# Kernel tuning notes

Hardware: AMD Instinct MI355X
Metric: run time of the kernel (lower is better)

The kernel has to match this reference:

```python
import jax, jax.numpy as jnp
import numpy as np

SEQ_LEN = 4096
D_IN = 2048
D_OUT = 2048
DROPOUT_P = 0.5


def setup_inputs() -> dict:
    key = jax.random.key(0)
    kx, kq, kk, kv = jax.random.split(key, 4)
    return {
        "x": jax.random.normal(kx, (SEQ_LEN, D_IN), dtype=jnp.float32),
        "W_query": jax.random.uniform(kq, (D_IN, D_OUT), dtype=jnp.float32),
        "W_key": jax.random.uniform(kk, (D_IN, D_OUT), dtype=jnp.float32),
        "W_value": jax.random.uniform(kv, (D_IN, D_OUT), dtype=jnp.float32),
    }


def reference(x, W_query, W_key, W_value):
    # projections: [S, d_in] @ [d_in, d_out] -> [S, d_out]
    queries = x @ W_query
    keys = x @ W_key
    values = x @ W_value
    # full score matrix [S, S]
    attn_scores = queries @ keys.T
    S = attn_scores.shape[0]
    causal_mask = jnp.triu(jnp.ones((S, S), dtype=bool), k=1)
    masked = jnp.where(causal_mask, -jnp.inf, attn_scores)
    scale = jnp.sqrt(jnp.asarray(keys.shape[-1], dtype=masked.dtype))
    attn_weights = jax.nn.softmax(masked / scale, axis=1)
    # dropout p=0.5 (train mode), inverted scaling, deterministic key
    keep = jax.random.bernoulli(jax.random.key(42), 1.0 - DROPOUT_P, attn_weights.shape)
    attn_weights = jnp.where(keep, attn_weights / (1.0 - DROPOUT_P), 0.0)
    context_vec = attn_weights @ values  # [S, d_out]
    return context_vec
```

## Files before the change

kernel.cpp:

```cpp
#include <hip/hip_runtime.h>
#include <cstdint>
#include <cstddef>
#include <cmath>

#define SEQ 4096
#define DM  2048

typedef unsigned int u32;
typedef unsigned short u16;
typedef __attribute__((ext_vector_type(8))) short bf16x8;
typedef __attribute__((ext_vector_type(4))) float f32x4;
typedef __attribute__((ext_vector_type(16))) float f32x16;

__device__ __forceinline__ u16 f2bf(float f) {
  u32 u = __float_as_uint(f);
  return (u16)((u + 0x7FFFu + ((u >> 16) & 1u)) >> 16);
}
__device__ __forceinline__ float bf2f(u16 h) { return __uint_as_float(((u32)h) << 16); }

__device__ __forceinline__ u32 rotl32(u32 x, int r) { return (x << r) | (x >> (32 - r)); }

__device__ __forceinline__ void tf2x32(u32 c0, u32 c1, u32& o0, u32& o1) {
  const u32 k0 = 0u, k1 = 42u, k2 = 0x1BD11BDAu ^ 0u ^ 42u;
  u32 x0 = c0 + k0;
  u32 x1 = c1 + k1;
#define TFR(r) { x0 += x1; x1 = rotl32(x1, (r)); x1 ^= x0; }
  TFR(13) TFR(15) TFR(26) TFR(6)   x0 += k1; x1 += k2 + 1u;
  TFR(17) TFR(29) TFR(16) TFR(24)  x0 += k2; x1 += k0 + 2u;
  TFR(13) TFR(15) TFR(26) TFR(6)   x0 += k0; x1 += k1 + 3u;
  TFR(17) TFR(29) TFR(16) TFR(24)  x0 += k1; x1 += k2 + 4u;
  TFR(13) TFR(15) TFR(26) TFR(6)   x0 += k2; x1 += k0 + 5u;
#undef TFR
  o0 = x0; o1 = x1;
}

__device__ __forceinline__ bool dropout_keep(u32 idx) {
  u32 a, b; tf2x32(0u, idx, a, b);
  return (((a ^ b) & 0x80000000u) == 0u);
}

__device__ __forceinline__ void g2l16(const void* g, void* l) {
  __builtin_amdgcn_global_load_lds((const __attribute__((address_space(1))) u32*)g,
                                   (__attribute__((address_space(3))) u32*)l, 16, 0, 0);
}

#define MFMA16(a, b, c) __builtin_amdgcn_mfma_f32_16x16x32_bf16(a, b, c, 0, 0, 0)
#define MFMA32(a, b, c) __builtin_amdgcn_mfma_f32_32x32x16_bf16(a, b, c, 0, 0, 0)


__device__ __forceinline__ void gemm_core(
    const u16* __restrict__ Ah, const u16* __restrict__ Bh,
    int lda, int ldb, int rowBlock, int colBlock, int kmax,
    f32x4 (&acc)[4][4], u16* smem)
{
  u16* Als = smem;
  u16* Bls = smem + 8192;
  const int tid  = threadIdx.x;
  const int wid  = tid >> 6;
  const int lane = tid & 63;
  const int wr   = (wid & 1) << 6;
  const int wc   = (wid >> 1) << 6;
  const int lrow = lane & 15;
  const int lk   = (((lane >> 4) ^ ((lrow >> 1) & 3)) << 3);
  const int srow = wid * 32 + (lane >> 2);
  const int skol = (((lane & 3) ^ ((lane >> 3) & 3)) << 3);

  const f32x4 zero = {0.f, 0.f, 0.f, 0.f};
#pragma unroll
  for (int i = 0; i < 4; ++i)
#pragma unroll
    for (int j = 0; j < 4; ++j) acc[i][j] = zero;

  for (int kb = 0; kb < kmax; kb += 64) {
#pragma unroll
    for (int h = 0; h < 2; ++h)
#pragma unroll
      for (int t = 0; t < 2; ++t) {
        const size_t ga = (size_t)(rowBlock + srow + t * 16) * lda + kb + h * 32 + skol;
        const size_t gb = (size_t)(colBlock + srow + t * 16) * ldb + kb + h * 32 + skol;
        const int lo = h * 4096 + (wid * 32 + t * 16) * 32;
        g2l16(Ah + ga, &Als[lo]);
        g2l16(Bh + gb, &Bls[lo]);
      }
    __syncthreads();

#pragma unroll
    for (int h = 0; h < 2; ++h) {
      bf16x8 ah[4], bh[4];
#pragma unroll
      for (int r = 0; r < 4; ++r) {
        ah[r] = *(const bf16x8*)&Als[h * 4096 + (wr + r * 16 + lrow) * 32 + lk];
        bh[r] = *(const bf16x8*)&Bls[h * 4096 + (wc + r * 16 + lrow) * 32 + lk];
      }
#pragma unroll
      for (int r = 0; r < 4; ++r)
#pragma unroll
        for (int c = 0; c < 4; ++c)
          acc[r][c] = MFMA16(ah[r], bh[c], acc[r][c]);
    }
    __syncthreads();
  }
}

__global__ __launch_bounds__(256) void k_split_all(
    const float* __restrict__ X, u16* __restrict__ Xh, u16* __restrict__ Xl,
    const float* __restrict__ Wq, const float* __restrict__ Wk, const float* __restrict__ Wv,
    u16* __restrict__ Wqh, u16* __restrict__ Wql,
    u16* __restrict__ Wkh, u16* __restrict__ Wkl, u16* __restrict__ Wvh) {
  __shared__ float t[64][65];
  const int bid = blockIdx.x;
  const int tid = threadIdx.x;
  const int wid = tid >> 6, lane = tid & 63;

  if (bid < 4096) {
    const int kt16 = bid & 127;
    const int rt32 = (bid >> 7) * 4 + wid;
    const int row = rt32 * 32 + (lane & 31);
    const int col = kt16 * 16 + ((lane >> 5) << 3);
    const float* src = X + (size_t)row * DM + col;
    const float4 v0 = *(const float4*)src;
    const float4 v1 = *(const float4*)(src + 4);
    float v[8] = {v0.x, v0.y, v0.z, v0.w, v1.x, v1.y, v1.z, v1.w};
    u16 h[8], l[8];
#pragma unroll
    for (int j = 0; j < 8; ++j) {
      h[j] = f2bf(v[j]);
      l[j] = f2bf(v[j] - bf2f(h[j]));
    }
    u16* hp = Xh + (size_t)row * DM + col;
    *(ushort4*)hp = *(ushort4*)&h[0];
    *(ushort4*)(hp + 4) = *(ushort4*)&h[4];
    u16* lp = Xl + (((size_t)rt32 * 128 + kt16) * 64 + lane) * 8;
    *(ushort4*)lp = *(ushort4*)&l[0];
    *(ushort4*)(lp + 4) = *(ushort4*)&l[4];
    return;
  }

  const int r = bid - 4096;
  const int z = r >> 10;
  const int rem = r & 1023;
  const int n0 = (rem & 31) * 64, k0 = (rem >> 5) * 64;
  const float* W = (z == 0) ? Wq : (z == 1) ? Wk : Wv;
  u16* Oh = (z == 0) ? Wqh : (z == 1) ? Wkh : Wvh;
  u16* Ol = (z == 0) ? Wql : Wkl;
  const int tx = tid & 63, ty = tid >> 6;
#pragma unroll
  for (int i = 0; i < 16; ++i)
    t[ty * 16 + i][tx] = W[(size_t)(k0 + ty * 16 + i) * DM + n0 + tx];
  __syncthreads();
  {
    const int nl = tid >> 2, kc = (tid & 3) * 16;
    u16 h[16];
#pragma unroll
    for (int i = 0; i < 16; ++i) h[i] = f2bf(t[kc + i][nl]);
    u16* hp = Oh + (size_t)(n0 + nl) * DM + k0 + kc;
#pragma unroll
    for (int i = 0; i < 4; ++i) *(ushort4*)(hp + i * 4) = *(ushort4*)&h[i * 4];
  }
  if (z < 2) {
#pragma unroll
    for (int tt = 0; tt < 2; ++tt) {
      const int idx = wid * 2 + tt;
      const int rt = idx >> 2, kt = idx & 3;
      const int nl = rt * 32 + (lane & 31);
      const int kc = kt * 16 + ((lane >> 5) << 3);
      u16 l[8];
#pragma unroll
      for (int j = 0; j < 8; ++j) {
        const float v = t[kc + j][nl];
        l[j] = f2bf(v - bf2f(f2bf(v)));
      }
      const int rtg = (n0 >> 5) + rt, ktg = (k0 >> 4) + kt;
      u16* lp = Ol + (((size_t)rtg * (DM / 16) + ktg) * 64 + lane) * 8;
      *(ushort4*)lp = *(ushort4*)&l[0];
      *(ushort4*)(lp + 4) = *(ushort4*)&l[4];
    }
  }
}

__global__ __launch_bounds__(512, 2) void k_proj_qk(
    const u16* __restrict__ Xh, const u16* __restrict__ Xl,
    const u16* __restrict__ Wqh, const u16* __restrict__ Wql,
    const u16* __restrict__ Wkh, const u16* __restrict__ Wkl,
    u16* __restrict__ Qh, u16* __restrict__ Ql,
    u16* __restrict__ Kh, u16* __restrict__ Kl, float rscaleQ)
{
  __shared__ __align__(16) u16 smem[65536];
  const int z = blockIdx.z;
  const u16* __restrict__ Bw = z ? Wkh : Wqh;
  const u16* __restrict__ Bl = z ? Wkl : Wql;
  u16* __restrict__ Oh = z ? Kh : Qh;
  u16* __restrict__ Ol = z ? Kl : Ql;
  const float rs = z ? 1.0f : rscaleQ;

  const int rowBlock = blockIdx.y * 256;
  const int colBlock = blockIdx.x * 256;
  const int tid  = threadIdx.x;
  const int wid  = tid >> 6, lane = tid & 63;
  const int wm   = wid >> 2, wn = wid & 3;
  const int l31  = lane & 31, lh = lane >> 5;
  const int srow = tid >> 2, schunk = tid & 3;
  const int sko  = ((schunk ^ ((srow >> 1) & 3)) << 3);
  const int rkey = (l31 >> 1) & 3;

  f32x16 acc[4][2];
  {
    const f32x16 z16 = {0.f,0.f,0.f,0.f,0.f,0.f,0.f,0.f,0.f,0.f,0.f,0.f,0.f,0.f,0.f,0.f};
#pragma unroll
    for (int r = 0; r < 4; ++r)
#pragma unroll
      for (int c = 0; c < 2; ++c) acc[r][c] = z16;
  }

#define P_STG_AHI(pp) g2l16(Xh + (size_t)(rowBlock + (pp)*128 + srow) * DM + kbn + sko, \
                            &smem[bufN + (pp)*4096 + tid*8]);
#define P_STG_BHI(pp) g2l16(Bw + (size_t)(colBlock + (pp)*128 + srow) * DM + kbn + sko, \
                            &smem[bufN + 8192 + (pp)*4096 + tid*8]);
#define P_STG_ALO(ss) { const int idx_ = (ss)*8 + wid; \
    g2l16(Xl + ((size_t)((rowBlock >> 5) + (idx_ >> 1)) * 128 + (kbn >> 4) + (idx_ & 1)) * 512 + lane*8, \
          &smem[bufN + 16384 + idx_*512 + lane*8]); }
#define P_STG_BLO(ss) { const int idx_ = (ss)*8 + wid; \
    g2l16(Bl + ((size_t)((colBlock >> 5) + (idx_ >> 1)) * 128 + (kbn >> 4) + (idx_ & 1)) * 512 + lane*8, \
          &smem[bufN + 24576 + idx_*512 + lane*8]); }

#define P_PHASE(qq) { \
    bf16x8 ah[4], bh[2], al[4], bl[2]; \
    const int cl_ = (qq)*2 + lh; \
    _Pragma("unroll") for (int r_ = 0; r_ < 4; ++r_) \
      ah[r_] = *(const bf16x8*)&smem[bufC + ((wm*128 + r_*32 + l31) << 5) + ((cl_ ^ rkey) << 3)]; \
    _Pragma("unroll") for (int c_ = 0; c_ < 2; ++c_) \
      bh[c_] = *(const bf16x8*)&smem[bufC + 8192 + ((wn*64 + c_*32 + l31) << 5) + ((cl_ ^ rkey) << 3)]; \
    _Pragma("unroll") for (int r_ = 0; r_ < 4; ++r_) \
      al[r_] = *(const bf16x8*)&smem[bufC + 16384 + ((wm*4 + r_)*2 + (qq))*512 + lane*8]; \
    _Pragma("unroll") for (int c_ = 0; c_ < 2; ++c_) \
      bl[c_] = *(const bf16x8*)&smem[bufC + 24576 + ((wn*2 + c_)*2 + (qq))*512 + lane*8]; \
    __builtin_amdgcn_s_setprio(1); \
    _Pragma("unroll") for (int r_ = 0; r_ < 4; ++r_) \
      _Pragma("unroll") for (int c_ = 0; c_ < 2; ++c_) { \
        acc[r_][c_] = MFMA32(ah[r_], bh[c_], acc[r_][c_]); \
        acc[r_][c_] = MFMA32(ah[r_], bl[c_], acc[r_][c_]); \
        acc[r_][c_] = MFMA32(al[r_], bh[c_], acc[r_][c_]); } \
    __builtin_amdgcn_s_setprio(0); }

  {
    const size_t kbn = 0; const int bufN = 0;
    P_STG_AHI(0) P_STG_AHI(1) P_STG_BHI(0) P_STG_BHI(1)
    P_STG_ALO(0) P_STG_ALO(1) P_STG_BLO(0) P_STG_BLO(1)
  }
  asm volatile("s_waitcnt vmcnt(0)" ::: "memory");
  __builtin_amdgcn_s_barrier();

  for (int t = 0; t < 64; ++t) {
    const int bufC = (t & 1) << 15;
    const int bufN = bufC ^ 32768;
    const size_t kbn = (size_t)(t + 1) * 32;
    if (t < 63) { P_STG_AHI(0) P_STG_AHI(1) P_STG_BHI(0) P_STG_BHI(1) }
    __builtin_amdgcn_sched_barrier(0);
    P_PHASE(0)
    if (t < 63) { P_STG_ALO(0) P_STG_ALO(1) P_STG_BLO(0) P_STG_BLO(1) }
    __builtin_amdgcn_sched_barrier(0);
    P_PHASE(1)
    asm volatile("s_waitcnt vmcnt(0)" ::: "memory");
    __builtin_amdgcn_s_barrier();
  }
#undef P_PHASE
#undef P_STG_BLO
#undef P_STG_ALO
#undef P_STG_BHI
#undef P_STG_AHI

  __syncthreads();
  u16* scr = smem + wid * 8192;
  const int r0g = rowBlock + wm * 128;
  const int c0g = colBlock + wn * 64;
#pragma unroll
  for (int r = 0; r < 4; ++r)
#pragma unroll
    for (int c = 0; c < 2; ++c) {
      const int colL = c * 32 + l31;
#pragma unroll
      for (int g = 0; g < 4; ++g)
#pragma unroll
        for (int e = 0; e < 4; ++e) {
          const int rowL = r * 32 + 8 * g + 4 * lh + e;
          const float v = acc[r][c][g * 4 + e] * rs;
          const u16 h = f2bf(v);
          Oh[(size_t)(r0g + rowL) * DM + c0g + colL] = h;
          scr[rowL * 64 + (((colL >> 3) ^ (rowL & 7)) << 3) + (colL & 7)] =
              f2bf(v - bf2f(h));
        }
    }
  asm volatile("s_waitcnt lgkmcnt(0)" ::: "memory");
  __builtin_amdgcn_sched_barrier(0);
#pragma unroll
  for (int rt = 0; rt < 4; ++rt)
#pragma unroll
    for (int kt = 0; kt < 4; ++kt) {
      const int rowL = rt * 32 + l31;
      const int cl2 = kt * 2 + lh;
      const bf16x8 v = *(const bf16x8*)&scr[rowL * 64 + ((cl2 ^ (rowL & 7)) << 3)];
      const int rtg = (rowBlock >> 5) + wm * 4 + rt;
      const int ktg = (colBlock >> 4) + wn * 4 + kt;
      *(bf16x8*)(Ol + (((size_t)rtg * 128 + ktg) * 64 + lane) * 8) = v;
    }
}

__global__ __launch_bounds__(512, 2) void k_proj_v(
    const u16* __restrict__ Xh, const u16* __restrict__ Wvh, u16* __restrict__ Vt)
{
  __shared__ __align__(16) u16 smem[49152];
  const int rowBlock = blockIdx.y * 256;
  const int colBlock = blockIdx.x * 128;
  const int tid  = threadIdx.x;
  const int wid  = tid >> 6, lane = tid & 63;
  const int wm   = wid >> 1, wn = wid & 1;
  const int l31  = lane & 31, lh = lane >> 5;
  const int srow = tid >> 2, schunk = tid & 3;
  const int sko  = ((schunk ^ ((srow >> 1) & 3)) << 3);
  const int rkey = (l31 >> 1) & 3;

  f32x16 acc[2][2];
  {
    const f32x16 z16 = {0.f,0.f,0.f,0.f,0.f,0.f,0.f,0.f,0.f,0.f,0.f,0.f,0.f,0.f,0.f,0.f};
#pragma unroll
    for (int r = 0; r < 2; ++r)
#pragma unroll
      for (int c = 0; c < 2; ++c) acc[r][c] = z16;
  }

#define V_STGA(hh, pp) g2l16(Xh + (size_t)(rowBlock + (pp)*128 + srow) * DM + kbn + (hh)*32 + sko, \
                             &smem[bufN + (hh)*8192 + (pp)*4096 + tid*8]);
#define V_STGB(hh)     g2l16(Wvh + (size_t)(colBlock + srow) * DM + kbn + (hh)*32 + sko, \
                             &smem[bufN + 16384 + (hh)*4096 + tid*8]);

#define V_PH(qq, STMT) { \
    __builtin_amdgcn_sched_barrier(0); \
    STMT; \
    bf16x8 ah[2], bh[2]; \
    const int cl_ = ((qq) & 1) * 2 + lh; \
    const int hx_ = (qq) >> 1; \
    _Pragma("unroll") for (int r_ = 0; r_ < 2; ++r_) \
      ah[r_] = *(const bf16x8*)&smem[bufC + ((hx_*256 + wm*64 + r_*32 + l31) << 5) + ((cl_ ^ rkey) << 3)]; \
    _Pragma("unroll") for (int c_ = 0; c_ < 2; ++c_) \
      bh[c_] = *(const bf16x8*)&smem[bufC + 16384 + ((hx_*128 + wn*64 + c_*32 + l31) << 5) + ((cl_ ^ rkey) << 3)]; \
    __builtin_amdgcn_s_setprio(1); \
    _Pragma("unroll") for (int r_ = 0; r_ < 2; ++r_) \
      _Pragma("unroll") for (int c_ = 0; c_ < 2; ++c_) \
        acc[r_][c_] = MFMA32(ah[r_], bh[c_], acc[r_][c_]); \
    __builtin_amdgcn_s_setprio(0); }

  {
    const size_t kbn = 0; const int bufN = 0;
    V_STGA(0,0) V_STGA(0,1) V_STGA(1,0) V_STGA(1,1) V_STGB(0) V_STGB(1)
  }
  asm volatile("s_waitcnt vmcnt(0)" ::: "memory");
  __builtin_amdgcn_s_barrier();

  for (int t = 0; t < 32; ++t) {
    const int bufC = (t & 1) * 24576;
    const int bufN = bufC ^ 24576;
    const size_t kbn = (size_t)(t + 1) * 64;
    const bool more = (t < 31);
    V_PH(0, if (more) { V_STGA(0,0) V_STGA(0,1) V_STGB(0) })
    V_PH(1, if (more) { V_STGA(1,0) V_STGA(1,1) V_STGB(1) })
    V_PH(2, ;)
    V_PH(3, ;)
    asm volatile("s_waitcnt vmcnt(0)" ::: "memory");
    __builtin_amdgcn_s_barrier();
  }
#undef V_PH
#undef V_STGB
#undef V_STGA

  const int vr0 = rowBlock + wm * 64;
#pragma unroll
  for (int r = 0; r < 2; ++r)
#pragma unroll
    for (int c = 0; c < 2; ++c) {
      const int col = colBlock + wn * 64 + c * 32 + l31;
#pragma unroll
      for (int g = 0; g < 4; ++g) {
        ushort4 pk;
        pk.x = f2bf(acc[r][c][g * 4 + 0]);
        pk.y = f2bf(acc[r][c][g * 4 + 1]);
        pk.z = f2bf(acc[r][c][g * 4 + 2]);
        pk.w = f2bf(acc[r][c][g * 4 + 3]);
        *(ushort4*)(Vt + (size_t)col * SEQ + vr0 + r * 32 + 8 * g + 4 * lh) = pk;
      }
    }
}

__global__ __launch_bounds__(512, 2) void k_scores(
    const u16* __restrict__ Qh, const u16* __restrict__ Ql,
    const u16* __restrict__ Kh, const u16* __restrict__ Kl, float* __restrict__ S)
{
  __shared__ __align__(16) u16 smem[49152];
  const int bid = blockIdx.x;
  int by = (int)((sqrtf(4.0f * (float)bid + 1.0f) - 1.0f) * 0.5f);
  while ((by + 1) * (by + 2) <= bid) ++by;
  while (by * (by + 1) > bid) --by;
  const int bx = bid - by * (by + 1);
  const int rowBlock = by * 256, colBlock = bx * 128;

  const int tid  = threadIdx.x;
  const int wid  = tid >> 6, lane = tid & 63;
  const int wm   = wid >> 1, wn = wid & 1;
  const int l31  = lane & 31, lh = lane >> 5;
  const int srow = tid >> 2, schunk = tid & 3;
  const int sko  = ((schunk ^ ((srow >> 1) & 3)) << 3);
  const int rkey = (l31 >> 1) & 3;

  f32x16 acc[2][2];
  {
    const f32x16 z16 = {0.f,0.f,0.f,0.f,0.f,0.f,0.f,0.f,0.f,0.f,0.f,0.f,0.f,0.f,0.f,0.f};
#pragma unroll
    for (int r = 0; r < 2; ++r)
#pragma unroll
      for (int c = 0; c < 2; ++c) acc[r][c] = z16;
  }

#define S_STG_AHI(pp) g2l16(Qh + (size_t)(rowBlock + (pp)*128 + srow) * DM + kbn + sko, \
                            &smem[bufN + (pp)*4096 + tid*8]);
#define S_STG_BHI     g2l16(Kh + (size_t)(colBlock + srow) * DM + kbn + sko, \
                            &smem[bufN + 8192 + tid*8]);
#define S_STG_ALO(ss) { const int idx_ = (ss)*8 + wid; \
    g2l16(Ql + ((size_t)((rowBlock >> 5) + (idx_ >> 1)) * 128 + (kbn >> 4) + (idx_ & 1)) * 512 + lane*8, \
          &smem[bufN + 12288 + idx_*512 + lane*8]); }
#define S_STG_BLO     { const int idx_ = wid; \
    g2l16(Kl + ((size_t)((colBlock >> 5) + (idx_ >> 1)) * 128 + (kbn >> 4) + (idx_ & 1)) * 512 + lane*8, \
          &smem[bufN + 20480 + idx_*512 + lane*8]); }

#define S_PHASE(qq) { \
    bf16x8 ah[2], bh[2], al[2], bl[2]; \
    const int cl_ = (qq)*2 + lh; \
    _Pragma("unroll") for (int r_ = 0; r_ < 2; ++r_) \
      ah[r_] = *(const bf16x8*)&smem[bufC + ((wm*64 + r_*32 + l31) << 5) + ((cl_ ^ rkey) << 3)]; \
    _Pragma("unroll") for (int c_ = 0; c_ < 2; ++c_) \
      bh[c_] = *(const bf16x8*)&smem[bufC + 8192 + ((wn*64 + c_*32 + l31) << 5) + ((cl_ ^ rkey) << 3)]; \
    _Pragma("unroll") for (int r_ = 0; r_ < 2; ++r_) \
      al[r_] = *(const bf16x8*)&smem[bufC + 12288 + ((wm*2 + r_)*2 + (qq))*512 + lane*8]; \
    _Pragma("unroll") for (int c_ = 0; c_ < 2; ++c_) \
      bl[c_] = *(const bf16x8*)&smem[bufC + 20480 + ((wn*2 + c_)*2 + (qq))*512 + lane*8]; \
    __builtin_amdgcn_s_setprio(1); \
    _Pragma("unroll") for (int r_ = 0; r_ < 2; ++r_) \
      _Pragma("unroll") for (int c_ = 0; c_ < 2; ++c_) { \
        acc[r_][c_] = MFMA32(ah[r_], bh[c_], acc[r_][c_]); \
        acc[r_][c_] = MFMA32(ah[r_], bl[c_], acc[r_][c_]); \
        acc[r_][c_] = MFMA32(al[r_], bh[c_], acc[r_][c_]); } \
    __builtin_amdgcn_s_setprio(0); }

  {
    const size_t kbn = 0; const int bufN = 0;
    S_STG_AHI(0) S_STG_AHI(1) S_STG_BHI
    S_STG_ALO(0) S_STG_ALO(1) S_STG_BLO
  }
  asm volatile("s_waitcnt vmcnt(0)" ::: "memory");
  __builtin_amdgcn_s_barrier();

  for (int t = 0; t < 64; ++t) {
    const int bufC = (t & 1) * 24576;
    const int bufN = bufC ^ 24576;
    const size_t kbn = (size_t)(t + 1) * 32;
    if (t < 63) { S_STG_AHI(0) S_STG_AHI(1) S_STG_BHI }
    __builtin_amdgcn_sched_barrier(0);
    S_PHASE(0)
    if (t < 63) { S_STG_ALO(0) S_STG_ALO(1) S_STG_BLO }
    __builtin_amdgcn_sched_barrier(0);
    S_PHASE(1)
    asm volatile("s_waitcnt vmcnt(0)" ::: "memory");
    __builtin_amdgcn_s_barrier();
  }
#undef S_PHASE
#undef S_STG_BLO
#undef S_STG_ALO
#undef S_STG_BHI
#undef S_STG_AHI

  const int r0 = rowBlock + wm * 64, c0 = colBlock + wn * 64;
#pragma unroll
  for (int r = 0; r < 2; ++r)
#pragma unroll
    for (int c = 0; c < 2; ++c) {
      const int col = c0 + c * 32 + l31;
#pragma unroll
      for (int g = 0; g < 4; ++g)
#pragma unroll
        for (int e = 0; e < 4; ++e) {
          const int row = r0 + r * 32 + 8 * g + 4 * lh + e;
          S[(size_t)row * SEQ + col] = acc[r][c][g * 4 + e];
        }
    }
}

__global__ __launch_bounds__(256) void k_softmax_dropout(const float* __restrict__ S,
                                                         u16* __restrict__ P) {
  const int row = blockIdx.x;
  const int n = row + 1;
  const int nt = (n + 1023) >> 10;
  const int tid = threadIdx.x;
  __shared__ float buf[SEQ];
  __shared__ float red[4];
  __shared__ float bcast;
  const float* srow = S + (size_t)row * SEQ;

  float lmax = -INFINITY;
  for (int t = 0; t < nt; ++t) {
    int j4 = tid + t * 256;
    float4 v = *(const float4*)(srow + (size_t)j4 * 4);
    int b = j4 * 4;
    float x0 = (b + 0 < n) ? v.x : -INFINITY;
    float x1 = (b + 1 < n) ? v.y : -INFINITY;
    float x2 = (b + 2 < n) ? v.z : -INFINITY;
    float x3 = (b + 3 < n) ? v.w : -INFINITY;
    buf[b + 0] = x0; buf[b + 1] = x1; buf[b + 2] = x2; buf[b + 3] = x3;
    lmax = fmaxf(lmax, fmaxf(fmaxf(x0, x1), fmaxf(x2, x3)));
  }
  for (int off = 32; off > 0; off >>= 1) lmax = fmaxf(lmax, __shfl_down(lmax, off, 64));
  if ((tid & 63) == 0) red[tid >> 6] = lmax;
  __syncthreads();
  if (tid == 0) bcast = fmaxf(fmaxf(red[0], red[1]), fmaxf(red[2], red[3]));
  __syncthreads();
  const float m = bcast;

  float lsum = 0.f;
  for (int t = 0; t < nt; ++t) {
    int b = (tid + t * 256) * 4;
    float e0 = expf(buf[b + 0] - m);
    float e1 = expf(buf[b + 1] - m);
    float e2 = expf(buf[b + 2] - m);
    float e3 = expf(buf[b + 3] - m);
    buf[b + 0] = e0; buf[b + 1] = e1; buf[b + 2] = e2; buf[b + 3] = e3;
    lsum += (e0 + e1) + (e2 + e3);
  }
  for (int off = 32; off > 0; off >>= 1) lsum += __shfl_down(lsum, off, 64);
  if ((tid & 63) == 0) red[tid >> 6] = lsum;
  __syncthreads();
  if (tid == 0) bcast = (red[0] + red[1]) + (red[2] + red[3]);
  __syncthreads();
  const float total = bcast;

  u16* prow = P + (size_t)row * SEQ;
  const int zeroEnd = ((row >> 7) + 1) << 7;
  for (int j = tid; j < zeroEnd; j += 256) {
    float out = 0.f;
    if (j < n) {
      const float w = buf[j] / total;
      out = dropout_keep((u32)(row * SEQ + j)) ? w * 2.0f : 0.f;
    }
    prow[j] = f2bf(out);
  }
}

__global__ __launch_bounds__(256) void k_pv(const u16* __restrict__ P,
                                            const u16* __restrict__ Vt,
                                            float* __restrict__ O) {
  __shared__ __align__(16) u16 smem[16384];
  const int by = (SEQ / 128 - 1) - blockIdx.y;
  f32x4 acc[4][4];
  gemm_core(P, Vt, SEQ, SEQ, by * 128, blockIdx.x * 128, (by + 1) * 128, acc, smem);

  const int lane = threadIdx.x & 63, wid = threadIdx.x >> 6;
  const int r0 = by * 128 + ((wid & 1) << 6) + ((lane >> 4) << 2);
  const int c0 = blockIdx.x * 128 + ((wid >> 1) << 6) + (lane & 15);
#pragma unroll
  for (int r = 0; r < 4; ++r)
#pragma unroll
    for (int c = 0; c < 4; ++c)
#pragma unroll
      for (int e = 0; e < 4; ++e)
        O[(size_t)(r0 + r * 16 + e) * DM + (c0 + c * 16)] = acc[r][c][e];
}

extern "C" void kernel_launch(void* const* d_in, const int* in_sizes, int n_in,
                              void* d_out, int out_size, void* d_ws, size_t ws_size,
                              hipStream_t stream) {
  const float* x  = (const float*)d_in[0];
  const float* Wq = (const float*)d_in[1];
  const float* Wk = (const float*)d_in[2];
  const float* Wv = (const float*)d_in[3];

  const size_t PL = (size_t)SEQ * DM;
  const size_t WL = (size_t)DM * DM;
  u16* base = (u16*)d_ws;
  u16* Qh = base;
  u16* Ql = Qh + PL;
  u16* Kh = Ql + PL;
  u16* Kl = Kh + PL;
  u16* Vt = Kl + PL;
  u16* P  = base;
  u16* regA = Vt + PL;
  u16* Xh  = regA;
  u16* Xl  = Xh + PL;
  u16* Wqh = Xl + PL;
  u16* Wql = Wqh + WL;
  u16* Wkh = Wql + WL;
  u16* Wkl = Wkh + WL;
  u16* Wvh = Wkl + WL;
  float* S = (float*)regA;

  const float rscale = 1.0f / sqrtf(2048.0f);
  k_split_all<<<dim3(4096 + 3 * 1024), dim3(256), 0, stream>>>(
      x, Xh, Xl, Wq, Wk, Wv, Wqh, Wql, Wkh, Wkl, Wvh);
  k_proj_qk<<<dim3(DM / 256, SEQ / 256, 2), dim3(512), 0, stream>>>(
      Xh, Xl, Wqh, Wql, Wkh, Wkl, Qh, Ql, Kh, Kl, rscale);
  k_proj_v<<<dim3(DM / 128, SEQ / 256), dim3(512), 0, stream>>>(Xh, Wvh, Vt);
  k_scores<<<dim3(272), dim3(512), 0, stream>>>(Qh, Ql, Kh, Kl, S);
  k_softmax_dropout<<<dim3(SEQ), dim3(256), 0, stream>>>(S, P);
  k_pv<<<dim3(DM / 128, SEQ / 128), dim3(256), 0, stream>>>(P, Vt, (float*)d_out);
}
```

Before: 610.4 us.

## Split K-tile loads by phase and use partial vmcnt waits in GEMMs

Reorganizes the global-to-LDS staging in the projection and score GEMM main loops. Each tile's loads are grouped by which MFMA phase consumes them, and each phase waits with a partial vmcnt count plus a barrier instead of draining all loads at the end of the iteration. The last iteration is peeled. The aim is to let phase 0 compute start before the phase-1 low-part loads arrive, keeping more loads in flight. In exchange there are more barriers per iteration, and the hardcoded vmcnt counts depend on exact issue order, so correctness is fragile.

```diff
diff --git a/kernel.cpp b/kernel.cpp
--- a/kernel.cpp
+++ b/kernel.cpp
@@ -212,16 +212,20 @@
       for (int c = 0; c < 2; ++c) acc[r][c] = z16;
   }
 
-#define P_STG_AHI(pp) g2l16(Xh + (size_t)(rowBlock + (pp)*128 + srow) * DM + kbn + sko, \
-                            &smem[bufN + (pp)*4096 + tid*8]);
-#define P_STG_BHI(pp) g2l16(Bw + (size_t)(colBlock + (pp)*128 + srow) * DM + kbn + sko, \
-                            &smem[bufN + 8192 + (pp)*4096 + tid*8]);
-#define P_STG_ALO(ss) { const int idx_ = (ss)*8 + wid; \
-    g2l16(Xl + ((size_t)((rowBlock >> 5) + (idx_ >> 1)) * 128 + (kbn >> 4) + (idx_ & 1)) * 512 + lane*8, \
-          &smem[bufN + 16384 + idx_*512 + lane*8]); }
-#define P_STG_BLO(ss) { const int idx_ = (ss)*8 + wid; \
-    g2l16(Bl + ((size_t)((colBlock >> 5) + (idx_ >> 1)) * 128 + (kbn >> 4) + (idx_ & 1)) * 512 + lane*8, \
-          &smem[bufN + 24576 + idx_*512 + lane*8]); }
+#define QK_G1 { \
+    g2l16(Xh + (size_t)(rowBlock + srow) * DM + kbn + sko,          &smem[bufN + tid*8]); \
+    g2l16(Xh + (size_t)(rowBlock + 128 + srow) * DM + kbn + sko,    &smem[bufN + 4096 + tid*8]); \
+    g2l16(Bw + (size_t)(colBlock + srow) * DM + kbn + sko,          &smem[bufN + 8192 + tid*8]); \
+    g2l16(Bw + (size_t)(colBlock + 128 + srow) * DM + kbn + sko,    &smem[bufN + 12288 + tid*8]); \
+    g2l16(Xl + ((size_t)((rowBlock >> 5) + wid) * 128 + (kbn >> 4)) * 512 + lane*8, \
+          &smem[bufN + 16384 + (wid*2)*512 + lane*8]); \
+    g2l16(Bl + ((size_t)((colBlock >> 5) + wid) * 128 + (kbn >> 4)) * 512 + lane*8, \
+          &smem[bufN + 24576 + (wid*2)*512 + lane*8]); }
+#define QK_G2 { \
+    g2l16(Xl + ((size_t)((rowBlock >> 5) + wid) * 128 + (kbn >> 4) + 1) * 512 + lane*8, \
+          &smem[bufN + 16384 + (wid*2+1)*512 + lane*8]); \
+    g2l16(Bl + ((size_t)((colBlock >> 5) + wid) * 128 + (kbn >> 4) + 1) * 512 + lane*8, \
+          &smem[bufN + 24576 + (wid*2+1)*512 + lane*8]); }
 
 #define P_PHASE(qq) { \
     bf16x8 ah[4], bh[2], al[4], bl[2]; \
@@ -244,30 +248,40 @@
 
   {
     const size_t kbn = 0; const int bufN = 0;
-    P_STG_AHI(0) P_STG_AHI(1) P_STG_BHI(0) P_STG_BHI(1)
-    P_STG_ALO(0) P_STG_ALO(1) P_STG_BLO(0) P_STG_BLO(1)
-  }
-  asm volatile("s_waitcnt vmcnt(0)" ::: "memory");
-  __builtin_amdgcn_s_barrier();
-
-  for (int t = 0; t < 64; ++t) {
+    QK_G1 QK_G2
+  }
+
+  for (int t = 0; t < 63; ++t) {
     const int bufC = (t & 1) << 15;
     const int bufN = bufC ^ 32768;
     const size_t kbn = (size_t)(t + 1) * 32;
-    if (t < 63) { P_STG_AHI(0) P_STG_AHI(1) P_STG_BHI(0) P_STG_BHI(1) }
-    __builtin_amdgcn_sched_barrier(0);
+    QK_G1
+    asm volatile("s_waitcnt vmcnt(8)" ::: "memory");
+    __builtin_amdgcn_s_barrier();
+    asm volatile("" ::: "memory");
     P_PHASE(0)
-    if (t < 63) { P_STG_ALO(0) P_STG_ALO(1) P_STG_BLO(0) P_STG_BLO(1) }
-    __builtin_amdgcn_sched_barrier(0);
+    QK_G2
+    asm volatile("s_waitcnt vmcnt(8)" ::: "memory");
+    __builtin_amdgcn_s_barrier();
+    asm volatile("" ::: "memory");
     P_PHASE(1)
+    asm volatile("" ::: "memory");
+    __builtin_amdgcn_s_barrier();
+  }
+  {
+    const int bufC = 32768;
+    asm volatile("s_waitcnt vmcnt(2)" ::: "memory");
+    __builtin_amdgcn_s_barrier();
+    asm volatile("" ::: "memory");
+    P_PHASE(0)
     asm volatile("s_waitcnt vmcnt(0)" ::: "memory");
     __builtin_amdgcn_s_barrier();
+    asm volatile("" ::: "memory");
+    P_PHASE(1)
   }
 #undef P_PHASE
-#undef P_STG_BLO
-#undef P_STG_ALO
-#undef P_STG_BHI
-#undef P_STG_AHI
+#undef QK_G2
+#undef QK_G1
 
   __syncthreads();
   u16* scr = smem + wid * 8192;
@@ -419,16 +433,19 @@
       for (int c = 0; c < 2; ++c) acc[r][c] = z16;
   }
 
-#define S_STG_AHI(pp) g2l16(Qh + (size_t)(rowBlock + (pp)*128 + srow) * DM + kbn + sko, \
-                            &smem[bufN + (pp)*4096 + tid*8]);
-#define S_STG_BHI     g2l16(Kh + (size_t)(colBlock + srow) * DM + kbn + sko, \
-                            &smem[bufN + 8192 + tid*8]);
-#define S_STG_ALO(ss) { const int idx_ = (ss)*8 + wid; \
-    g2l16(Ql + ((size_t)((rowBlock >> 5) + (idx_ >> 1)) * 128 + (kbn >> 4) + (idx_ & 1)) * 512 + lane*8, \
-          &smem[bufN + 12288 + idx_*512 + lane*8]); }
-#define S_STG_BLO     { const int idx_ = wid; \
-    g2l16(Kl + ((size_t)((colBlock >> 5) + (idx_ >> 1)) * 128 + (kbn >> 4) + (idx_ & 1)) * 512 + lane*8, \
-          &smem[bufN + 20480 + idx_*512 + lane*8]); }
+#define S_G1 { \
+    g2l16(Qh + (size_t)(rowBlock + srow) * DM + kbn + sko,        &smem[bufN + tid*8]); \
+    g2l16(Qh + (size_t)(rowBlock + 128 + srow) * DM + kbn + sko,  &smem[bufN + 4096 + tid*8]); \
+    g2l16(Kh + (size_t)(colBlock + srow) * DM + kbn + sko,        &smem[bufN + 8192 + tid*8]); \
+    g2l16(Ql + ((size_t)((rowBlock >> 5) + wid) * 128 + (kbn >> 4)) * 512 + lane*8, \
+          &smem[bufN + 12288 + (wid*2)*512 + lane*8]); \
+    g2l16(Kl + ((size_t)((colBlock >> 5) + (wid & 3)) * 128 + (kbn >> 4)) * 512 + lane*8, \
+          &smem[bufN + 20480 + ((wid & 3)*2)*512 + lane*8]); }
+#define S_G2 { \
+    g2l16(Ql + ((size_t)((rowBlock >> 5) + wid) * 128 + (kbn >> 4) + 1) * 512 + lane*8, \
+          &smem[bufN + 12288 + (wid*2+1)*512 + lane*8]); \
+    g2l16(Kl + ((size_t)((colBlock >> 5) + (wid & 3)) * 128 + (kbn >> 4) + 1) * 512 + lane*8, \
+          &smem[bufN + 20480 + ((wid & 3)*2+1)*512 + lane*8]); }
 
 #define S_PHASE(qq) { \
     bf16x8 ah[2], bh[2], al[2], bl[2]; \
@@ -451,30 +468,40 @@
 
   {
     const size_t kbn = 0; const int bufN = 0;
-    S_STG_AHI(0) S_STG_AHI(1) S_STG_BHI
-    S_STG_ALO(0) S_STG_ALO(1) S_STG_BLO
-  }
-  asm volatile("s_waitcnt vmcnt(0)" ::: "memory");
-  __builtin_amdgcn_s_barrier();
-
-  for (int t = 0; t < 64; ++t) {
+    S_G1 S_G2
+  }
+
+  for (int t = 0; t < 63; ++t) {
     const int bufC = (t & 1) * 24576;
     const int bufN = bufC ^ 24576;
     const size_t kbn = (size_t)(t + 1) * 32;
-    if (t < 63) { S_STG_AHI(0) S_STG_AHI(1) S_STG_BHI }
-    __builtin_amdgcn_sched_barrier(0);
+    S_G1
+    asm volatile("s_waitcnt vmcnt(7)" ::: "memory");
+    __builtin_amdgcn_s_barrier();
+    asm volatile("" ::: "memory");
     S_PHASE(0)
-    if (t < 63) { S_STG_ALO(0) S_STG_ALO(1) S_STG_BLO }
-    __builtin_amdgcn_sched_barrier(0);
+    S_G2
+    asm volatile("s_waitcnt vmcnt(7)" ::: "memory");
+    __builtin_amdgcn_s_barrier();
+    asm volatile("" ::: "memory");
     S_PHASE(1)
+    asm volatile("" ::: "memory");
+    __builtin_amdgcn_s_barrier();
+  }
+  {
+    const int bufC = 24576;
+    asm volatile("s_waitcnt vmcnt(2)" ::: "memory");
+    __builtin_amdgcn_s_barrier();
+    asm volatile("" ::: "memory");
+    S_PHASE(0)
     asm volatile("s_waitcnt vmcnt(0)" ::: "memory");
     __builtin_amdgcn_s_barrier();
+    asm volatile("" ::: "memory");
+    S_PHASE(1)
   }
 #undef S_PHASE
-#undef S_STG_BLO
-#undef S_STG_ALO
-#undef S_STG_BHI
-#undef S_STG_AHI
+#undef S_G2
+#undef S_G1
 
   const int r0 = rowBlock + wm * 64, c0 = colBlock + wn * 64;
 #pragma unroll
```

After: 634.7 us. 1.04x slower.

## Shrink QK projection and score tiles, stage K16 slices per warp with higher occupancy

Applied to the files above, without the earlier changes.

Tiles shrink in two kernels: the Q/K projection goes from 256x256 to 128x256 and the causal score kernel from 256x128 to 128x128, with the triangular block mapping recomputed for the new grid. Staging now uses per-warp pointers that advance through K in 16-wide steps with simple strided loads into unswizzled shared memory. This cuts shared memory per block and raises the occupancy hint (4 blocks per CU), aiming to hide latency better and reduce wasted work on the causal diagonal. The cost is less operand reuse per block, twice as many loop iterations with a barrier each, and possible bank conflicts, since the swizzling was dropped and high-part rows are now read with a plain lane stride.

```diff
diff --git a/kernel.cpp b/kernel.cpp
--- a/kernel.cpp
+++ b/kernel.cpp
@@ -178,103 +178,93 @@
   }
 }
 
-__global__ __launch_bounds__(512, 2) void k_proj_qk(
+__global__ __launch_bounds__(512, 4) void k_proj_qk(
     const u16* __restrict__ Xh, const u16* __restrict__ Xl,
     const u16* __restrict__ Wqh, const u16* __restrict__ Wql,
     const u16* __restrict__ Wkh, const u16* __restrict__ Wkl,
     u16* __restrict__ Qh, u16* __restrict__ Ql,
     u16* __restrict__ Kh, u16* __restrict__ Kl, float rscaleQ)
 {
-  __shared__ __align__(16) u16 smem[65536];
+  __shared__ __align__(16) u16 smem[32768];
   const int z = blockIdx.z;
   const u16* __restrict__ Bw = z ? Wkh : Wqh;
-  const u16* __restrict__ Bl = z ? Wkl : Wql;
+  const u16* __restrict__ Blg = z ? Wkl : Wql;
   u16* __restrict__ Oh = z ? Kh : Qh;
   u16* __restrict__ Ol = z ? Kl : Ql;
   const float rs = z ? 1.0f : rscaleQ;
 
-  const int rowBlock = blockIdx.y * 256;
+  const int rowBlock = blockIdx.y * 128;
   const int colBlock = blockIdx.x * 256;
   const int tid  = threadIdx.x;
   const int wid  = tid >> 6, lane = tid & 63;
   const int wm   = wid >> 2, wn = wid & 3;
   const int l31  = lane & 31, lh = lane >> 5;
-  const int srow = tid >> 2, schunk = tid & 3;
-  const int sko  = ((schunk ^ ((srow >> 1) & 3)) << 3);
-  const int rkey = (l31 >> 1) & 3;
-
-  f32x16 acc[4][2];
+
+  const u16* srcA;
+  size_t stepA;
+  if (wid < 4) {
+    srcA  = Xh + (size_t)(rowBlock + wid * 32 + l31) * DM + lh * 8;
+    stepA = 16;
+  } else {
+    srcA  = Xl + (size_t)((rowBlock >> 5) + (wid - 4)) * 128 * 512 + lane * 8;
+    stepA = 512;
+  }
+  const u16* srcBh = Bw  + (size_t)(colBlock + wid * 32 + l31) * DM + lh * 8;
+  const u16* srcBl = Blg + (size_t)((colBlock >> 5) + wid) * 128 * 512 + lane * 8;
+
+  f32x16 acc[2][2];
   {
     const f32x16 z16 = {0.f,0.f,0.f,0.f,0.f,0.f,0.f,0.f,0.f,0.f,0.f,0.f,0.f,0.f,0.f,0.f};
 #pragma unroll
-    for (int r = 0; r < 4; ++r)
+    for (int r = 0; r < 2; ++r)
 #pragma unroll
       for (int c = 0; c < 2; ++c) acc[r][c] = z16;
   }
 
-#define P_STG_AHI(pp) g2l16(Xh + (size_t)(rowBlock + (pp)*128 + srow) * DM + kbn + sko, \
-                            &smem[bufN + (pp)*4096 + tid*8]);
-#define P_STG_BHI(pp) g2l16(Bw + (size_t)(colBlock + (pp)*128 + srow) * DM + kbn + sko, \
-                            &smem[bufN + 8192 + (pp)*4096 + tid*8]);
-#define P_STG_ALO(ss) { const int idx_ = (ss)*8 + wid; \
-    g2l16(Xl + ((size_t)((rowBlock >> 5) + (idx_ >> 1)) * 128 + (kbn >> 4) + (idx_ & 1)) * 512 + lane*8, \
-          &smem[bufN + 16384 + idx_*512 + lane*8]); }
-#define P_STG_BLO(ss) { const int idx_ = (ss)*8 + wid; \
-    g2l16(Bl + ((size_t)((colBlock >> 5) + (idx_ >> 1)) * 128 + (kbn >> 4) + (idx_ & 1)) * 512 + lane*8, \
-          &smem[bufN + 24576 + idx_*512 + lane*8]); }
-
-#define P_PHASE(qq) { \
-    bf16x8 ah[4], bh[2], al[4], bl[2]; \
-    const int cl_ = (qq)*2 + lh; \
-    _Pragma("unroll") for (int r_ = 0; r_ < 4; ++r_) \
-      ah[r_] = *(const bf16x8*)&smem[bufC + ((wm*128 + r_*32 + l31) << 5) + ((cl_ ^ rkey) << 3)]; \
-    _Pragma("unroll") for (int c_ = 0; c_ < 2; ++c_) \
-      bh[c_] = *(const bf16x8*)&smem[bufC + 8192 + ((wn*64 + c_*32 + l31) << 5) + ((cl_ ^ rkey) << 3)]; \
-    _Pragma("unroll") for (int r_ = 0; r_ < 4; ++r_) \
-      al[r_] = *(const bf16x8*)&smem[bufC + 16384 + ((wm*4 + r_)*2 + (qq))*512 + lane*8]; \
-    _Pragma("unroll") for (int c_ = 0; c_ < 2; ++c_) \
-      bl[c_] = *(const bf16x8*)&smem[bufC + 24576 + ((wn*2 + c_)*2 + (qq))*512 + lane*8]; \
+#define P_STG(bufN) { \
+    g2l16(srcA,  &smem[(bufN) + tid * 8]); \
+    g2l16(srcBh, &smem[(bufN) + 4096 + tid * 8]); \
+    g2l16(srcBl, &smem[(bufN) + 8192 + tid * 8]); \
+    srcA += stepA; srcBh += 16; srcBl += 512; }
+
+#define P_PH(bufC) { \
+    bf16x8 ah[2], bh[2], al[2], bl[2]; \
+    _Pragma("unroll") for (int r_ = 0; r_ < 2; ++r_) { \
+      ah[r_] = *(const bf16x8*)&smem[(bufC) + (wm*2 + r_)*512 + lane*8]; \
+      al[r_] = *(const bf16x8*)&smem[(bufC) + 2048 + (wm*2 + r_)*512 + lane*8]; } \
+    _Pragma("unroll") for (int c_ = 0; c_ < 2; ++c_) { \
+      bh[c_] = *(const bf16x8*)&smem[(bufC) + 4096 + (wn*2 + c_)*512 + lane*8]; \
+      bl[c_] = *(const bf16x8*)&smem[(bufC) + 8192 + (wn*2 + c_)*512 + lane*8]; } \
     __builtin_amdgcn_s_setprio(1); \
-    _Pragma("unroll") for (int r_ = 0; r_ < 4; ++r_) \
+    _Pragma("unroll") for (int r_ = 0; r_ < 2; ++r_) \
       _Pragma("unroll") for (int c_ = 0; c_ < 2; ++c_) { \
         acc[r_][c_] = MFMA32(ah[r_], bh[c_], acc[r_][c_]); \
         acc[r_][c_] = MFMA32(ah[r_], bl[c_], acc[r_][c_]); \
         acc[r_][c_] = MFMA32(al[r_], bh[c_], acc[r_][c_]); } \
     __builtin_amdgcn_s_setprio(0); }
 
-  {
-    const size_t kbn = 0; const int bufN = 0;
-    P_STG_AHI(0) P_STG_AHI(1) P_STG_BHI(0) P_STG_BHI(1)
-    P_STG_ALO(0) P_STG_ALO(1) P_STG_BLO(0) P_STG_BLO(1)
-  }
+  P_STG(0)
   asm volatile("s_waitcnt vmcnt(0)" ::: "memory");
   __builtin_amdgcn_s_barrier();
 
-  for (int t = 0; t < 64; ++t) {
-    const int bufC = (t & 1) << 15;
-    const int bufN = bufC ^ 32768;
-    const size_t kbn = (size_t)(t + 1) * 32;
-    if (t < 63) { P_STG_AHI(0) P_STG_AHI(1) P_STG_BHI(0) P_STG_BHI(1) }
+  for (int t = 0; t < 128; ++t) {
+    const int bufC = (t & 1) * 12288;
+    const int bufN = bufC ^ 12288;
+    if (t < 127) P_STG(bufN)
     __builtin_amdgcn_sched_barrier(0);
-    P_PHASE(0)
-    if (t < 63) { P_STG_ALO(0) P_STG_ALO(1) P_STG_BLO(0) P_STG_BLO(1) }
-    __builtin_amdgcn_sched_barrier(0);
-    P_PHASE(1)
+    P_PH(bufC)
     asm volatile("s_waitcnt vmcnt(0)" ::: "memory");
     __builtin_amdgcn_s_barrier();
   }
-#undef P_PHASE
-#undef P_STG_BLO
-#undef P_STG_ALO
-#undef P_STG_BHI
-#undef P_STG_AHI
+#undef P_PH
+#undef P_STG
 
   __syncthreads();
-  u16* scr = smem + wid * 8192;
-  const int r0g = rowBlock + wm * 128;
+  u16* scr = smem + wid * 4096;
+  const int r0g = rowBlock + wm * 64;
   const int c0g = colBlock + wn * 64;
 #pragma unroll
-  for (int r = 0; r < 4; ++r)
+  for (int r = 0; r < 2; ++r)
 #pragma unroll
     for (int c = 0; c < 2; ++c) {
       const int colL = c * 32 + l31;
@@ -293,13 +283,13 @@
   asm volatile("s_waitcnt lgkmcnt(0)" ::: "memory");
   __builtin_amdgcn_sched_barrier(0);
 #pragma unroll
-  for (int rt = 0; rt < 4; ++rt)
+  for (int rt = 0; rt < 2; ++rt)
 #pragma unroll
     for (int kt = 0; kt < 4; ++kt) {
       const int rowL = rt * 32 + l31;
       const int cl2 = kt * 2 + lh;
       const bf16x8 v = *(const bf16x8*)&scr[rowL * 64 + ((cl2 ^ (rowL & 7)) << 3)];
-      const int rtg = (rowBlock >> 5) + wm * 4 + rt;
+      const int rtg = (rowBlock >> 5) + wm * 2 + rt;
       const int ktg = (colBlock >> 4) + wn * 4 + kt;
       *(bf16x8*)(Ol + (((size_t)rtg * 128 + ktg) * 64 + lane) * 8) = v;
     }
@@ -390,25 +380,27 @@
     }
 }
 
-__global__ __launch_bounds__(512, 2) void k_scores(
+__global__ __launch_bounds__(256, 4) void k_scores(
     const u16* __restrict__ Qh, const u16* __restrict__ Ql,
     const u16* __restrict__ Kh, const u16* __restrict__ Kl, float* __restrict__ S)
 {
-  __shared__ __align__(16) u16 smem[49152];
+  __shared__ __align__(16) u16 smem[16384];
   const int bid = blockIdx.x;
-  int by = (int)((sqrtf(4.0f * (float)bid + 1.0f) - 1.0f) * 0.5f);
-  while ((by + 1) * (by + 2) <= bid) ++by;
-  while (by * (by + 1) > bid) --by;
-  const int bx = bid - by * (by + 1);
-  const int rowBlock = by * 256, colBlock = bx * 128;
+  int by = (int)((sqrtf(8.0f * (float)bid + 1.0f) - 1.0f) * 0.5f);
+  while ((by + 1) * (by + 2) / 2 <= bid) ++by;
+  while (by * (by + 1) / 2 > bid) --by;
+  const int bx = bid - by * (by + 1) / 2;
+  const int rowBlock = by * 128, colBlock = bx * 128;
 
   const int tid  = threadIdx.x;
   const int wid  = tid >> 6, lane = tid & 63;
   const int wm   = wid >> 1, wn = wid & 1;
   const int l31  = lane & 31, lh = lane >> 5;
-  const int srow = tid >> 2, schunk = tid & 3;
-  const int sko  = ((schunk ^ ((srow >> 1) & 3)) << 3);
-  const int rkey = (l31 >> 1) & 3;
+
+  const u16* srcAh = Qh + (size_t)(rowBlock + wid * 32 + l31) * DM + lh * 8;
+  const u16* srcAl = Ql + (size_t)((rowBlock >> 5) + wid) * 128 * 512 + lane * 8;
+  const u16* srcBh = Kh + (size_t)(colBlock + wid * 32 + l31) * DM + lh * 8;
+  const u16* srcBl = Kl + (size_t)((colBlock >> 5) + wid) * 128 * 512 + lane * 8;
 
   f32x16 acc[2][2];
   {
@@ -419,28 +411,21 @@
       for (int c = 0; c < 2; ++c) acc[r][c] = z16;
   }
 
-#define S_STG_AHI(pp) g2l16(Qh + (size_t)(rowBlock + (pp)*128 + srow) * DM + kbn + sko, \
-                            &smem[bufN + (pp)*4096 + tid*8]);
-#define S_STG_BHI     g2l16(Kh + (size_t)(colBlock + srow) * DM + kbn + sko, \
-                            &smem[bufN + 8192 + tid*8]);
-#define S_STG_ALO(ss) { const int idx_ = (ss)*8 + wid; \
-    g2l16(Ql + ((size_t)((rowBlock >> 5) + (idx_ >> 1)) * 128 + (kbn >> 4) + (idx_ & 1)) * 512 + lane*8, \
-          &smem[bufN + 12288 + idx_*512 + lane*8]); }
-#define S_STG_BLO     { const int idx_ = wid; \
-    g2l16(Kl + ((size_t)((colBlock >> 5) + (idx_ >> 1)) * 128 + (kbn >> 4) + (idx_ & 1)) * 512 + lane*8, \
-          &smem[bufN + 20480 + idx_*512 + lane*8]); }
-
-#define S_PHASE(qq) { \
+#define S_STG(bufN) { \
+    g2l16(srcAh, &smem[(bufN) + tid * 8]); \
+    g2l16(srcAl, &smem[(bufN) + 2048 + tid * 8]); \
+    g2l16(srcBh, &smem[(bufN) + 4096 + tid * 8]); \
+    g2l16(srcBl, &smem[(bufN) + 6144 + tid * 8]); \
+    srcAh += 16; srcAl += 512; srcBh += 16; srcBl += 512; }
+
+#define S_PH(bufC) { \
     bf16x8 ah[2], bh[2], al[2], bl[2]; \
-    const int cl_ = (qq)*2 + lh; \
-    _Pragma("unroll") for (int r_ = 0; r_ < 2; ++r_) \
-      ah[r_] = *(const bf16x8*)&smem[bufC + ((wm*64 + r_*32 + l31) << 5) + ((cl_ ^ rkey) << 3)]; \
-    _Pragma("unroll") for (int c_ = 0; c_ < 2; ++c_) \
-      bh[c_] = *(const bf16x8*)&smem[bufC + 8192 + ((wn*64 + c_*32 + l31) << 5) + ((cl_ ^ rkey) << 3)]; \
-    _Pragma("unroll") for (int r_ = 0; r_ < 2; ++r_) \
-      al[r_] = *(const bf16x8*)&smem[bufC + 12288 + ((wm*2 + r_)*2 + (qq))*512 + lane*8]; \
-    _Pragma("unroll") for (int c_ = 0; c_ < 2; ++c_) \
-      bl[c_] = *(const bf16x8*)&smem[bufC + 20480 + ((wn*2 + c_)*2 + (qq))*512 + lane*8]; \
+    _Pragma("unroll") for (int r_ = 0; r_ < 2; ++r_) { \
+      ah[r_] = *(const bf16x8*)&smem[(bufC) + (wm*2 + r_)*512 + lane*8]; \
+      al[r_] = *(const bf16x8*)&smem[(bufC) + 2048 + (wm*2 + r_)*512 + lane*8]; } \
+    _Pragma("unroll") for (int c_ = 0; c_ < 2; ++c_) { \
+      bh[c_] = *(const bf16x8*)&smem[(bufC) + 4096 + (wn*2 + c_)*512 + lane*8]; \
+      bl[c_] = *(const bf16x8*)&smem[(bufC) + 6144 + (wn*2 + c_)*512 + lane*8]; } \
     __builtin_amdgcn_s_setprio(1); \
     _Pragma("unroll") for (int r_ = 0; r_ < 2; ++r_) \
       _Pragma("unroll") for (int c_ = 0; c_ < 2; ++c_) { \
@@ -449,32 +434,21 @@
         acc[r_][c_] = MFMA32(al[r_], bh[c_], acc[r_][c_]); } \
     __builtin_amdgcn_s_setprio(0); }
 
-  {
-    const size_t kbn = 0; const int bufN = 0;
-    S_STG_AHI(0) S_STG_AHI(1) S_STG_BHI
-    S_STG_ALO(0) S_STG_ALO(1) S_STG_BLO
-  }
+  S_STG(0)
   asm volatile("s_waitcnt vmcnt(0)" ::: "memory");
   __builtin_amdgcn_s_barrier();
 
-  for (int t = 0; t < 64; ++t) {
-    const int bufC = (t & 1) * 24576;
-    const int bufN = bufC ^ 24576;
-    const size_t kbn = (size_t)(t + 1) * 32;
-    if (t < 63) { S_STG_AHI(0) S_STG_AHI(1) S_STG_BHI }
+  for (int t = 0; t < 128; ++t) {
+    const int bufC = (t & 1) * 8192;
+    const int bufN = bufC ^ 8192;
+    if (t < 127) S_STG(bufN)
     __builtin_amdgcn_sched_barrier(0);
-    S_PHASE(0)
-    if (t < 63) { S_STG_ALO(0) S_STG_ALO(1) S_STG_BLO }
-    __builtin_amdgcn_sched_barrier(0);
-    S_PHASE(1)
+    S_PH(bufC)
     asm volatile("s_waitcnt vmcnt(0)" ::: "memory");
     __builtin_amdgcn_s_barrier();
   }
-#undef S_PHASE
-#undef S_STG_BLO
-#undef S_STG_ALO
-#undef S_STG_BHI
-#undef S_STG_AHI
+#undef S_PH
+#undef S_STG
 
   const int r0 = rowBlock + wm * 64, c0 = colBlock + wn * 64;
 #pragma unroll
@@ -601,10 +575,11 @@
   const float rscale = 1.0f / sqrtf(2048.0f);
   k_split_all<<<dim3(4096 + 3 * 1024), dim3(256), 0, stream>>>(
       x, Xh, Xl, Wq, Wk, Wv, Wqh, Wql, Wkh, Wkl, Wvh);
-  k_proj_qk<<<dim3(DM / 256, SEQ / 256, 2), dim3(512), 0, stream>>>(
+  k_proj_qk<<<dim3(DM / 256, SEQ / 128, 2), dim3(512), 0, stream>>>(
       Xh, Xl, Wqh, Wql, Wkh, Wkl, Qh, Ql, Kh, Kl, rscale);
   k_proj_v<<<dim3(DM / 128, SEQ / 256), dim3(512), 0, stream>>>(Xh, Wvh, Vt);
-  k_scores<<<dim3(272), dim3(512), 0, stream>>>(Qh, Ql, Kh, Kl, S);
+  k_scores<<<dim3((SEQ / 128) * (SEQ / 128 + 1) / 2), dim3(256), 0, stream>>>(
+      Qh, Ql, Kh, Kl, S);
   k_softmax_dropout<<<dim3(SEQ), dim3(256), 0, stream>>>(S, P);
   k_pv<<<dim3(DM / 128, SEQ / 128), dim3(256), 0, stream>>>(P, Vt, (float*)d_out);
 }
```

Measured after the change: 643.6 us. +5.4%, slower.
